# Performance work log

Hardware: AMD Instinct MI355X
Metric: run time of the kernel (lower is better)

Reference implementation:

```python
import jax, jax.numpy as jnp
import numpy as np

GS = 256      # grid/node count
PARAM = 128   # feature width
KC = 32       # keepconst (constant features)
I1, I2 = 64, 32
PK = PARAM - KC
K_DIV = 16.0  # neighbor-count normalizer
EPS = 1e-3    # Keras BatchNorm default epsilon
B = 4


def _bn(x, g, b, m, v):
    # inference-mode batch norm over last axis
    return (x - m) * jax.lax.rsqrt(v + EPS) * g + b


def setup_inputs() -> dict:
    key = jax.random.key(0)
    ks = jax.random.split(key, 24)
    mat = (jax.random.uniform(ks[0], (B, GS, GS)) < (K_DIV / GS)).astype(jnp.float32)
    val = jax.random.normal(ks[1], (B, GS, PARAM), dtype=jnp.float32)
    def w(k, shape):
        fan = shape[0] if len(shape) > 1 else shape[0]
        return jax.random.normal(k, shape, dtype=jnp.float32) * (1.0 / np.sqrt(fan))
    inp = {
        'mat': mat, 'val': val,
        'M1': w(ks[2], (2 * PARAM, I1)), 'B1': 0.05 * jax.random.normal(ks[3], (I1,)),
        'M2': w(ks[4], (I1, I2)),        'B2': 0.05 * jax.random.normal(ks[5], (I2,)),
        'M3': w(ks[6], (I2, PK)),        'B3': 0.05 * jax.random.normal(ks[7], (PK,)),
    }
    for idx, d in zip((1, 2, 3), (I1, I2, PK)):
        kk = jax.random.split(ks[7 + idx], 4)
        inp[f'g{idx}'] = 1.0 + 0.1 * jax.random.normal(kk[0], (d,), dtype=jnp.float32)
        inp[f'b{idx}'] = 0.1 * jax.random.normal(kk[1], (d,), dtype=jnp.float32)
        inp[f'm{idx}'] = 0.1 * jax.random.normal(kk[2], (d,), dtype=jnp.float32)
        inp[f'v{idx}'] = jax.random.uniform(kk[3], (d,), dtype=jnp.float32, minval=0.5, maxval=1.5)
    return inp


def reference(mat, val, M1, B1, M2, B2, M3, B3,
              g1, b1, m1, v1, g2, b2, m2, v2, g3, b3, m3, v3):
    con = val[:, :, :KC]
    # selector matmuls == gather: pair i -> (a=i//GS, b=i%GS)
    feat = jnp.repeat(val, GS, axis=1)          # (B, GS*GS, PARAM) = val_a
    vb = jnp.tile(val, (1, GS, 1))              # (B, GS*GS, PARAM) = val_b
    premlp = jnp.concatenate([feat, vb - feat], axis=-1)  # (B, GS*GS, 2*PARAM)
    s = jax.nn.relu(_bn(premlp @ M1 + B1, g1, b1, m1, v1))
    s = jax.nn.relu(_bn(s @ M2 + B2, g2, b2, m2, v2))
    s = jax.nn.relu(_bn(s @ M3 + B3, g3, b3, m3, v3))      # (B, GS*GS, PK)
    res = s.reshape(val.shape[0], GS, GS, PK)               # (B, a, b, PK)
    # masked scatter-sum over neighbor axis b
    summ = jnp.einsum('babk,bab->bak'.replace('a', 'x').replace('b', 'y', 1), res, mat) if False else \
        jnp.einsum('bxyk,bxy->bxk', res, mat)               # (B, GS, PK)
    var = jnp.clip(summ / K_DIV, -1.0, 1.0)                 # advrelu([-1,1]) == clip
    return jnp.concatenate([con, var], axis=-1)             # (B, GS, PARAM)
```

## Files before the change

### kernel.cpp

```cpp
#include <hip/hip_runtime.h>

#define GS    256
#define PARAM 128
#define KC    32
#define I1    64
#define I2    32
#define PK    96
#define B_    4
#define NROWS (B_ * GS)
#define EPS   1e-3f
#define KDIV_INV (1.0f / 16.0f)

constexpr int U_OFF   = 0;
constexpr int W_OFF   = NROWS * I1;
constexpr int M2F_OFF = 2 * NROWS * I1;
constexpr int C2_OFF  = M2F_OFF + I1 * I2;
constexpr int M3F_OFF = C2_OFF + I2;
constexpr int C3_OFF  = M3F_OFF + I2 * PK;
constexpr int C1_OFF  = C3_OFF + PK;

__device__ __forceinline__ float rdlane(float v, int l) {
    return __uint_as_float(__builtin_amdgcn_readlane(__float_as_uint(v), l));
}

__global__ __launch_bounds__(256) void glmlp_precompute(
    const float* __restrict__ val, const float* __restrict__ M1,
    const float* __restrict__ B1,
    const float* __restrict__ M2, const float* __restrict__ B2,
    const float* __restrict__ M3, const float* __restrict__ B3,
    const float* __restrict__ g1, const float* __restrict__ b1,
    const float* __restrict__ m1, const float* __restrict__ v1,
    const float* __restrict__ g2, const float* __restrict__ b2,
    const float* __restrict__ m2, const float* __restrict__ v2,
    const float* __restrict__ g3, const float* __restrict__ b3,
    const float* __restrict__ m3, const float* __restrict__ v3,
    float* __restrict__ ws, float* __restrict__ out)
{
    const int blk = blockIdx.x;
    const int t = threadIdx.x;

    if (blk < NROWS) {
        __shared__ float vrow[PARAM];
        __shared__ float red[4][I1];
        const int r = blk;
        if (t < PARAM) vrow[t] = val[r * PARAM + t];
        if (t < KC) out[r * PARAM + t] = val[r * PARAM + t];
        __syncthreads();

        const int i = t & (I1 - 1);
        const int q = t >> 6;
        const float* __restrict__ Mb = M1 + ((q >> 1) ? (PARAM * I1) : 0);
        const int p0 = (q & 1) * 64;
        float aa = 0.f, bb = 0.f;
        #pragma unroll 8
        for (int p = 0; p < 64; p += 2) {
            aa = fmaf(vrow[p0 + p],     Mb[(p0 + p) * I1 + i],     aa);
            bb = fmaf(vrow[p0 + p + 1], Mb[(p0 + p + 1) * I1 + i], bb);
        }
        red[q][i] = aa + bb;
        __syncthreads();

        if (q == 0) {
            const float T  = red[0][i] + red[1][i];
            const float Wv = red[2][i] + red[3][i];
            const float s1 = g1[i] * rsqrtf(v1[i] + EPS);
            ws[U_OFF + r * I1 + i] = (T - Wv) * s1;
            ws[W_OFF + r * I1 + i] = Wv * s1;
        }
    } else {
        if (t < I1) {
            const float s1 = g1[t] * rsqrtf(v1[t] + EPS);
            ws[C1_OFF + t] = B1[t] * s1 + b1[t] - m1[t] * s1;
        }
        if (t < I2) {
            const float s2 = g2[t] * rsqrtf(v2[t] + EPS);
            ws[C2_OFF + t] = B2[t] * s2 + b2[t] - m2[t] * s2;
        }
        if (t < PK) {
            const float s3 = g3[t] * rsqrtf(v3[t] + EPS);
            ws[C3_OFF + t] = B3[t] * s3 + b3[t] - m3[t] * s3;
        }
        for (int idx = t; idx < I1 * I2; idx += 256) {
            const int j = idx & (I2 - 1);
            const float s2 = g2[j] * rsqrtf(v2[j] + EPS);
            ws[M2F_OFF + idx] = M2[idx] * s2;
        }
        for (int idx = t; idx < I2 * PK; idx += 256) {
            const int k = idx % PK;
            const float s3 = g3[k] * rsqrtf(v3[k] + EPS);
            ws[M3F_OFF + idx] = M3[idx] * s3;
        }
    }
}

__global__ __launch_bounds__(256) void glmlp_pairs(
    const float* __restrict__ mat, const float* __restrict__ ws,
    float* __restrict__ out)
{
    __shared__ int   acty[GS];
    __shared__ float partial[4][PK];
    __shared__ int   cnt;

    const int r = blockIdx.x;
    const int t = threadIdx.x;
    const int lane = t & 63;
    const int w = t >> 6;
    const int jj = lane & 31;
    const int wbase = r & ~(GS - 1);
    const float* __restrict__ W = ws + W_OFF;

    if (t == 0) cnt = 0;
    const float mv = mat[r * GS + t];

    float m2col[I1];
    #pragma unroll
    for (int s = 0; s < I1; ++s)
        m2col[s] = ws[M2F_OFF + s * I2 + jj];
    float m3a[I2], m3b[I2];
    #pragma unroll
    for (int i = 0; i < I2; ++i) {
        m3a[i] = ws[M3F_OFF + i * PK + lane];
        m3b[i] = ws[M3F_OFF + i * PK + 64 + jj];
    }
    const float ux  = ws[U_OFF + r * I1 + lane] + ws[C1_OFF + lane];
    const float c2j = ws[C2_OFF + jj];
    const float c30 = ws[C3_OFF + lane];
    const float c31 = ws[C3_OFF + 64 + jj];

    __syncthreads();
    if (mv != 0.0f) acty[atomicAdd(&cnt, 1)] = t;
    __syncthreads();
    const int n = cnt;

    float acc0 = 0.f, acc1 = 0.f;

    int p = w;
    float wv = (p < n) ? W[(wbase + acty[p]) * I1 + lane] : 0.f;
    while (p < n) {
        const int pn = p + 4;
        const float wvn = (pn < n) ? W[(wbase + acty[pn]) * I1 + lane] : 0.f;

        const float h1 = fmaxf(ux + wv, 0.f);

        float a0 = 0.f, a1 = 0.f, a2 = 0.f, a3 = 0.f;
        #pragma unroll
        for (int s = 0; s < I1; s += 4) {
            a0 = fmaf(rdlane(h1, s + 0), m2col[s + 0], a0);
            a1 = fmaf(rdlane(h1, s + 1), m2col[s + 1], a1);
            a2 = fmaf(rdlane(h1, s + 2), m2col[s + 2], a2);
            a3 = fmaf(rdlane(h1, s + 3), m2col[s + 3], a3);
        }
        const float h2 = fmaxf((a0 + a1) + (a2 + a3) + c2j, 0.f);

        float d0a = c30, d0b = 0.f, d1a = c31, d1b = 0.f;
        #pragma unroll
        for (int i = 0; i < I2; i += 2) {
            const float he = rdlane(h2, i);
            const float ho = rdlane(h2, i + 1);
            d0a = fmaf(he, m3a[i],     d0a);
            d0b = fmaf(ho, m3a[i + 1], d0b);
            d1a = fmaf(he, m3b[i],     d1a);
            d1b = fmaf(ho, m3b[i + 1], d1b);
        }
        acc0 += fmaxf(d0a + d0b, 0.f);
        acc1 += fmaxf(d1a + d1b, 0.f);

        wv = wvn;
        p = pn;
    }

    partial[w][lane] = acc0;
    if (lane < 32) partial[w][64 + lane] = acc1;
    __syncthreads();

    if (t < PK) {
        float v = (partial[0][t] + partial[1][t] + partial[2][t] + partial[3][t])
                  * KDIV_INV;
        v = fminf(fmaxf(v, -1.0f), 1.0f);
        out[r * PARAM + KC + t] = v;
    }
}

extern "C" void kernel_launch(void* const* d_in, const int* in_sizes, int n_in,
                              void* d_out, int out_size, void* d_ws, size_t ws_size,
                              hipStream_t stream) {
    const float* mat = (const float*)d_in[0];
    const float* val = (const float*)d_in[1];
    const float* M1  = (const float*)d_in[2];
    const float* B1  = (const float*)d_in[3];
    const float* M2  = (const float*)d_in[4];
    const float* B2  = (const float*)d_in[5];
    const float* M3  = (const float*)d_in[6];
    const float* B3  = (const float*)d_in[7];
    const float* g1  = (const float*)d_in[8];
    const float* b1  = (const float*)d_in[9];
    const float* m1  = (const float*)d_in[10];
    const float* v1  = (const float*)d_in[11];
    const float* g2  = (const float*)d_in[12];
    const float* b2  = (const float*)d_in[13];
    const float* m2  = (const float*)d_in[14];
    const float* v2  = (const float*)d_in[15];
    const float* g3  = (const float*)d_in[16];
    const float* b3  = (const float*)d_in[17];
    const float* m3  = (const float*)d_in[18];
    const float* v3  = (const float*)d_in[19];

    float* ws  = (float*)d_ws;
    float* out = (float*)d_out;

    hipLaunchKernelGGL(glmlp_precompute, dim3(NROWS + 1), dim3(256), 0, stream,
                       val, M1, B1, M2, B2, M3, B3,
                       g1, b1, m1, v1, g2, b2, m2, v2, g3, b3, m3, v3,
                       ws, out);

    hipLaunchKernelGGL(glmlp_pairs, dim3(NROWS), dim3(256), 0, stream,
                       mat, ws, out);
}
```

Before: 111.8 us.

## Fuse precompute and pair kernels into one cooperative launch with grid sync

Merges the two kernels into a single persistent kernel launched cooperatively, with a grid-wide barrier between the per-row M1 projection and the pair MLP phase. Folding of the BN scales into M2/M3 and the bias constants now happens per block in registers, which removes the separate constants block and its workspace round trip. The intent is to save a kernel launch and the inter-kernel gap. The cost is grid-sync overhead, redundant per-block folding, and fewer resident blocks under launch_bounds(256,3). If the cooperative launch fails, it falls back to two launches selected by a phase argument.

New measurement: 171.0 us. +52.9%, slower.

```diff
diff --git a/kernel.cpp b/kernel.cpp
--- a/kernel.cpp
+++ b/kernel.cpp
@@ -1,4 +1,7 @@
 #include <hip/hip_runtime.h>
+#include <hip/hip_cooperative_groups.h>
+
+namespace cg = cooperative_groups;
 
 #define GS    256
 #define PARAM 128
@@ -11,21 +14,16 @@
 #define EPS   1e-3f
 #define KDIV_INV (1.0f / 16.0f)
 
-constexpr int U_OFF   = 0;
-constexpr int W_OFF   = NROWS * I1;
-constexpr int M2F_OFF = 2 * NROWS * I1;
-constexpr int C2_OFF  = M2F_OFF + I1 * I2;
-constexpr int M3F_OFF = C2_OFF + I2;
-constexpr int C3_OFF  = M3F_OFF + I2 * PK;
-constexpr int C1_OFF  = C3_OFF + PK;
+constexpr int U_OFF = 0;
+constexpr int W_OFF = NROWS * I1;
 
 __device__ __forceinline__ float rdlane(float v, int l) {
     return __uint_as_float(__builtin_amdgcn_readlane(__float_as_uint(v), l));
 }
 
-__global__ __launch_bounds__(256) void glmlp_precompute(
-    const float* __restrict__ val, const float* __restrict__ M1,
-    const float* __restrict__ B1,
+__global__ __launch_bounds__(256, 3) void glmlp_fused(
+    const float* __restrict__ mat, const float* __restrict__ val,
+    const float* __restrict__ M1, const float* __restrict__ B1,
     const float* __restrict__ M2, const float* __restrict__ B2,
     const float* __restrict__ M3, const float* __restrict__ B3,
     const float* __restrict__ g1, const float* __restrict__ b1,
@@ -34,150 +32,134 @@
     const float* __restrict__ m2, const float* __restrict__ v2,
     const float* __restrict__ g3, const float* __restrict__ b3,
     const float* __restrict__ m3, const float* __restrict__ v3,
-    float* __restrict__ ws, float* __restrict__ out)
+    float* __restrict__ ws, float* __restrict__ out, int phase)
 {
-    const int blk = blockIdx.x;
-    const int t = threadIdx.x;
-
-    if (blk < NROWS) {
-        __shared__ float vrow[PARAM];
-        __shared__ float red[4][I1];
-        const int r = blk;
-        if (t < PARAM) vrow[t] = val[r * PARAM + t];
-        if (t < KC) out[r * PARAM + t] = val[r * PARAM + t];
-        __syncthreads();
-
-        const int i = t & (I1 - 1);
-        const int q = t >> 6;
-        const float* __restrict__ Mb = M1 + ((q >> 1) ? (PARAM * I1) : 0);
-        const int p0 = (q & 1) * 64;
-        float aa = 0.f, bb = 0.f;
-        #pragma unroll 8
-        for (int p = 0; p < 64; p += 2) {
-            aa = fmaf(vrow[p0 + p],     Mb[(p0 + p) * I1 + i],     aa);
-            bb = fmaf(vrow[p0 + p + 1], Mb[(p0 + p + 1) * I1 + i], bb);
-        }
-        red[q][i] = aa + bb;
-        __syncthreads();
-
-        if (q == 0) {
-            const float T  = red[0][i] + red[1][i];
-            const float Wv = red[2][i] + red[3][i];
-            const float s1 = g1[i] * rsqrtf(v1[i] + EPS);
-            ws[U_OFF + r * I1 + i] = (T - Wv) * s1;
-            ws[W_OFF + r * I1 + i] = Wv * s1;
-        }
-    } else {
-        if (t < I1) {
-            const float s1 = g1[t] * rsqrtf(v1[t] + EPS);
-            ws[C1_OFF + t] = B1[t] * s1 + b1[t] - m1[t] * s1;
-        }
-        if (t < I2) {
-            const float s2 = g2[t] * rsqrtf(v2[t] + EPS);
-            ws[C2_OFF + t] = B2[t] * s2 + b2[t] - m2[t] * s2;
-        }
-        if (t < PK) {
-            const float s3 = g3[t] * rsqrtf(v3[t] + EPS);
-            ws[C3_OFF + t] = B3[t] * s3 + b3[t] - m3[t] * s3;
-        }
-        for (int idx = t; idx < I1 * I2; idx += 256) {
-            const int j = idx & (I2 - 1);
-            const float s2 = g2[j] * rsqrtf(v2[j] + EPS);
-            ws[M2F_OFF + idx] = M2[idx] * s2;
-        }
-        for (int idx = t; idx < I2 * PK; idx += 256) {
-            const int k = idx % PK;
-            const float s3 = g3[k] * rsqrtf(v3[k] + EPS);
-            ws[M3F_OFF + idx] = M3[idx] * s3;
-        }
-    }
-}
-
-__global__ __launch_bounds__(256) void glmlp_pairs(
-    const float* __restrict__ mat, const float* __restrict__ ws,
-    float* __restrict__ out)
-{
+    __shared__ float vrow[PARAM];
+    __shared__ float red[4][I1];
     __shared__ int   acty[GS];
     __shared__ float partial[4][PK];
     __shared__ int   cnt;
 
-    const int r = blockIdx.x;
-    const int t = threadIdx.x;
+    const int nb   = gridDim.x;
+    const int t    = threadIdx.x;
     const int lane = t & 63;
-    const int w = t >> 6;
-    const int jj = lane & 31;
-    const int wbase = r & ~(GS - 1);
-    const float* __restrict__ W = ws + W_OFF;
-
-    if (t == 0) cnt = 0;
-    const float mv = mat[r * GS + t];
-
-    float m2col[I1];
-    #pragma unroll
-    for (int s = 0; s < I1; ++s)
-        m2col[s] = ws[M2F_OFF + s * I2 + jj];
-    float m3a[I2], m3b[I2];
-    #pragma unroll
-    for (int i = 0; i < I2; ++i) {
-        m3a[i] = ws[M3F_OFF + i * PK + lane];
-        m3b[i] = ws[M3F_OFF + i * PK + 64 + jj];
-    }
-    const float ux  = ws[U_OFF + r * I1 + lane] + ws[C1_OFF + lane];
-    const float c2j = ws[C2_OFF + jj];
-    const float c30 = ws[C3_OFF + lane];
-    const float c31 = ws[C3_OFF + 64 + jj];
-
-    __syncthreads();
-    if (mv != 0.0f) acty[atomicAdd(&cnt, 1)] = t;
-    __syncthreads();
-    const int n = cnt;
-
-    float acc0 = 0.f, acc1 = 0.f;
-
-    int p = w;
-    float wv = (p < n) ? W[(wbase + acty[p]) * I1 + lane] : 0.f;
-    while (p < n) {
-        const int pn = p + 4;
-        const float wvn = (pn < n) ? W[(wbase + acty[pn]) * I1 + lane] : 0.f;
-
-        const float h1 = fmaxf(ux + wv, 0.f);
-
-        float a0 = 0.f, a1 = 0.f, a2 = 0.f, a3 = 0.f;
+    const int w    = t >> 6;
+    const int jj   = lane & 31;
+
+    if (phase != 2) {
+        for (int r = blockIdx.x; r < NROWS; r += nb) {
+            if (t < PARAM) vrow[t] = val[r * PARAM + t];
+            if (t < KC)    out[r * PARAM + t] = val[r * PARAM + t];
+            __syncthreads();
+
+            const int i = lane;
+            const int q = w;
+            const float* __restrict__ Mb = M1 + ((q >> 1) ? (PARAM * I1) : 0);
+            const int p0 = (q & 1) * 64;
+            float aa = 0.f, bb = 0.f;
+            #pragma unroll 8
+            for (int p = 0; p < 64; p += 2) {
+                aa = fmaf(vrow[p0 + p],     Mb[(p0 + p) * I1 + i],     aa);
+                bb = fmaf(vrow[p0 + p + 1], Mb[(p0 + p + 1) * I1 + i], bb);
+            }
+            red[q][i] = aa + bb;
+            __syncthreads();
+
+            if (q == 0) {
+                const float T  = red[0][i] + red[1][i];
+                const float Wv = red[2][i] + red[3][i];
+                const float s1 = g1[i] * rsqrtf(v1[i] + EPS);
+                ws[U_OFF + r * I1 + i] = (T - Wv) * s1;
+                ws[W_OFF + r * I1 + i] = Wv * s1;
+            }
+        }
+    }
+
+    if (phase == 0) cg::this_grid().sync();
+
+    if (phase != 1) {
+        const float s2  = g2[jj] * rsqrtf(v2[jj] + EPS);
+        float m2col[I1];
         #pragma unroll
-        for (int s = 0; s < I1; s += 4) {
-            a0 = fmaf(rdlane(h1, s + 0), m2col[s + 0], a0);
-            a1 = fmaf(rdlane(h1, s + 1), m2col[s + 1], a1);
-            a2 = fmaf(rdlane(h1, s + 2), m2col[s + 2], a2);
-            a3 = fmaf(rdlane(h1, s + 3), m2col[s + 3], a3);
+        for (int s = 0; s < I1; ++s)
+            m2col[s] = M2[s * I2 + jj] * s2;
+
+        const float s3a = g3[lane]    * rsqrtf(v3[lane]    + EPS);
+        const float s3b = g3[64 + jj] * rsqrtf(v3[64 + jj] + EPS);
+        float m3a[I2], m3b[I2];
+        #pragma unroll
+        for (int k = 0; k < I2; ++k) {
+            m3a[k] = M3[k * PK + lane]    * s3a;
+            m3b[k] = M3[k * PK + 64 + jj] * s3b;
         }
-        const float h2 = fmaxf((a0 + a1) + (a2 + a3) + c2j, 0.f);
-
-        float d0a = c30, d0b = 0.f, d1a = c31, d1b = 0.f;
-        #pragma unroll
-        for (int i = 0; i < I2; i += 2) {
-            const float he = rdlane(h2, i);
-            const float ho = rdlane(h2, i + 1);
-            d0a = fmaf(he, m3a[i],     d0a);
-            d0b = fmaf(ho, m3a[i + 1], d0b);
-            d1a = fmaf(he, m3b[i],     d1a);
-            d1b = fmaf(ho, m3b[i + 1], d1b);
+
+        const float s1l = g1[lane] * rsqrtf(v1[lane] + EPS);
+        const float c1l = B1[lane] * s1l + b1[lane] - m1[lane] * s1l;
+        const float c2j = B2[jj]   * s2  + b2[jj]   - m2[jj]   * s2;
+        const float c30 = B3[lane]    * s3a + b3[lane]    - m3[lane]    * s3a;
+        const float c31 = B3[64 + jj] * s3b + b3[64 + jj] - m3[64 + jj] * s3b;
+
+        const float* __restrict__ W = ws + W_OFF;
+
+        for (int r = blockIdx.x; r < NROWS; r += nb) {
+            const int wbase = r & ~(GS - 1);
+            if (t == 0) cnt = 0;
+            __syncthreads();
+            const float mv = mat[r * GS + t];
+            if (mv != 0.0f) acty[atomicAdd(&cnt, 1)] = t;
+            const float ux = ws[U_OFF + r * I1 + lane] + c1l;
+            __syncthreads();
+            const int n = cnt;
+
+            float acc0 = 0.f, acc1 = 0.f;
+
+            int p = w;
+            float wv = (p < n) ? W[(wbase + acty[p]) * I1 + lane] : 0.f;
+            while (p < n) {
+                const int pn = p + 4;
+                const float wvn = (pn < n) ? W[(wbase + acty[pn]) * I1 + lane] : 0.f;
+
+                const float h1 = fmaxf(ux + wv, 0.f);
+
+                float a0 = 0.f, a1 = 0.f, a2 = 0.f, a3 = 0.f;
+                #pragma unroll
+                for (int s = 0; s < I1; s += 4) {
+                    a0 = fmaf(rdlane(h1, s + 0), m2col[s + 0], a0);
+                    a1 = fmaf(rdlane(h1, s + 1), m2col[s + 1], a1);
+                    a2 = fmaf(rdlane(h1, s + 2), m2col[s + 2], a2);
+                    a3 = fmaf(rdlane(h1, s + 3), m2col[s + 3], a3);
+                }
+                const float h2 = fmaxf((a0 + a1) + (a2 + a3) + c2j, 0.f);
+
+                float d0a = c30, d0b = 0.f, d1a = c31, d1b = 0.f;
+                #pragma unroll
+                for (int k = 0; k < I2; k += 2) {
+                    const float he = rdlane(h2, k);
+                    const float ho = rdlane(h2, k + 1);
+                    d0a = fmaf(he, m3a[k],     d0a);
+                    d0b = fmaf(ho, m3a[k + 1], d0b);
+                    d1a = fmaf(he, m3b[k],     d1a);
+                    d1b = fmaf(ho, m3b[k + 1], d1b);
+                }
+                acc0 += fmaxf(d0a + d0b, 0.f);
+                acc1 += fmaxf(d1a + d1b, 0.f);
+
+                wv = wvn;
+                p = pn;
+            }
+
+            partial[w][lane] = acc0;
+            if (lane < 32) partial[w][64 + lane] = acc1;
+            __syncthreads();
+
+            if (t < PK) {
+                float v = (partial[0][t] + partial[1][t] +
+                           partial[2][t] + partial[3][t]) * KDIV_INV;
+                v = fminf(fmaxf(v, -1.0f), 1.0f);
+                out[r * PARAM + KC + t] = v;
+            }
+            __syncthreads();
         }
-        acc0 += fmaxf(d0a + d0b, 0.f);
-        acc1 += fmaxf(d1a + d1b, 0.f);
-
-        wv = wvn;
-        p = pn;
-    }
-
-    partial[w][lane] = acc0;
-    if (lane < 32) partial[w][64 + lane] = acc1;
-    __syncthreads();
-
-    if (t < PK) {
-        float v = (partial[0][t] + partial[1][t] + partial[2][t] + partial[3][t])
-                  * KDIV_INV;
-        v = fminf(fmaxf(v, -1.0f), 1.0f);
-        out[r * PARAM + KC + t] = v;
     }
 }
 
@@ -208,11 +190,37 @@
     float* ws  = (float*)d_ws;
     float* out = (float*)d_out;
 
-    hipLaunchKernelGGL(glmlp_precompute, dim3(NROWS + 1), dim3(256), 0, stream,
-                       val, M1, B1, M2, B2, M3, B3,
-                       g1, b1, m1, v1, g2, b2, m2, v2, g3, b3, m3, v3,
-                       ws, out);
-
-    hipLaunchKernelGGL(glmlp_pairs, dim3(NROWS), dim3(256), 0, stream,
-                       mat, ws, out);
+    int occ = 0;
+    hipError_t qe = hipOccupancyMaxActiveBlocksPerMultiprocessor(
+        &occ, (const void*)glmlp_fused, 256, 0);
+    bool try_coop = (qe == hipSuccess) && (occ >= 1);
+    int grid = 256 * (occ < 1 ? 1 : occ);
+    if (grid > NROWS) grid = NROWS;
+
+    hipError_t le = hipErrorUnknown;
+    if (try_coop) {
+        int phase0 = 0;
+        void* args[] = {
+            (void*)&mat, (void*)&val, (void*)&M1, (void*)&B1,
+            (void*)&M2,  (void*)&B2,  (void*)&M3, (void*)&B3,
+            (void*)&g1, (void*)&b1, (void*)&m1, (void*)&v1,
+            (void*)&g2, (void*)&b2, (void*)&m2, (void*)&v2,
+            (void*)&g3, (void*)&b3, (void*)&m3, (void*)&v3,
+            (void*)&ws, (void*)&out, (void*)&phase0
+        };
+        le = hipLaunchCooperativeKernel((const void*)glmlp_fused,
+                                        dim3(grid), dim3(256), args, 0, stream);
+    }
+
+    if (le != hipSuccess) {
+        (void)hipGetLastError();
+        hipLaunchKernelGGL(glmlp_fused, dim3(NROWS), dim3(256), 0, stream,
+                           mat, val, M1, B1, M2, B2, M3, B3,
+                           g1, b1, m1, v1, g2, b2, m2, v2, g3, b3, m3, v3,
+                           ws, out, 1);
+        hipLaunchKernelGGL(glmlp_fused, dim3(NROWS), dim3(256), 0, stream,
+                           mat, val, M1, B1, M2, B2, M3, B3,
+                           g1, b1, m1, v1, g2, b2, m2, v2, g3, b3, m3, v3,
+                           ws, out, 2);
+    }
 }
```
